# Optimization experiments

Hardware: AMD Instinct MI355X
Metric: run time of the kernel (lower is better)

## Reference

```python
import jax, jax.numpy as jnp
import numpy as np

D = 1024

def setup_inputs() -> dict:
    key = jax.random.key(0)
    ks = jax.random.split(key, 7)
    s = 1.0 / np.sqrt(D)
    x = jax.random.normal(ks[0], (4, 4096, D), dtype=jnp.float32)
    Wq = jax.random.uniform(ks[1], (D, D), jnp.float32, -s, s)
    bq = jax.random.uniform(ks[2], (D,), jnp.float32, -s, s)
    Wk = jax.random.uniform(ks[3], (D, D), jnp.float32, -s, s)
    bk = jax.random.uniform(ks[4], (D,), jnp.float32, -s, s)
    Wv = jax.random.uniform(ks[5], (D, D), jnp.float32, -s, s)
    bv = jax.random.uniform(ks[6], (D,), jnp.float32, -s, s)
    return {"x": x, "Wq": Wq, "bq": bq, "Wk": Wk, "bk": bk, "Wv": Wv, "bv": bv}

def reference(x, Wq, bq, Wk, bk, Wv, bv):
    # nn.Linear: y = x @ W.T + b
    q = (jnp.einsum('bnd,ed->bne', x, Wq) + bq) / jnp.sqrt(jnp.float32(Wq.shape[0]))
    k = jnp.einsum('bnd,ed->bne', x, Wk) + bk
    v = jnp.einsum('bnd,ed->bne', x, Wv) + bv
    scores = jnp.einsum('bqd,bkd->bqk', q, k)  # [B,N,N]
    N = scores.shape[-1]
    mask = jnp.triu(jnp.full((N, N), -1e9, dtype=scores.dtype), k=1)
    probs = jax.nn.softmax(scores + mask, axis=-1)
    return jnp.einsum('bqk,bkd->bqd', probs, v)
```

## Files before the change

kernel.cpp:

```cpp
#include <hip/hip_runtime.h>
#include <hip/hip_bf16.h>
#include <stdint.h>


typedef __attribute__((ext_vector_type(8))) short short8;
typedef __attribute__((ext_vector_type(4))) float float4v;

__device__ inline unsigned short f2b(float f) {
  union { float f; unsigned u; } v; v.f = f;
  unsigned r = (v.u + 0x7fffu + ((v.u >> 16) & 1u)) >> 16;
  return (unsigned short)r;
}
__device__ inline float b2f(unsigned short b) {
  union { unsigned u; float f; } v; v.u = ((unsigned)b) << 16;
  return v.f;
}

typedef const __attribute__((address_space(1))) unsigned int* gptr_t;
typedef __attribute__((address_space(3))) unsigned int* lptr_t;

__device__ inline void gload_lds16(const unsigned short* g, unsigned short* l) {
  __builtin_amdgcn_global_load_lds((gptr_t)(const void*)g, (lptr_t)(void*)l, 16, 0, 0);
}

__global__ __launch_bounds__(256) void cvt_all(const float* __restrict__ x,
                                               const float* __restrict__ wq,
                                               const float* __restrict__ wk,
                                               const float* __restrict__ wv,
                                               unsigned short* __restrict__ xb,
                                               unsigned short* __restrict__ wb) {
  const float* src;
  unsigned short* dst;
  long n, i0, stride;
  if (blockIdx.x < 2048) {
    src = x; dst = xb; n = 16384L * 1024;
    i0 = ((long)blockIdx.x * 256 + threadIdx.x) * 4;
    stride = 2048L * 256 * 4;
  } else {
    int wsec = (blockIdx.x - 2048) >> 8;
    int blk = (blockIdx.x - 2048) & 255;
    src = wsec == 0 ? wq : (wsec == 1 ? wk : wv);
    dst = wb + (long)wsec * 1024 * 1024;
    n = 1024L * 1024;
    i0 = ((long)blk * 256 + threadIdx.x) * 4;
    stride = 256L * 256 * 4;
  }
  for (long i = i0; i < n; i += stride) {
    float4 f = *(const float4*)&src[i];
    union { unsigned short u[4]; uint2 v; } o;
    o.u[0] = f2b(f.x); o.u[1] = f2b(f.y); o.u[2] = f2b(f.z); o.u[3] = f2b(f.w);
    *(uint2*)&dst[i] = o.v;
  }
}

__device__ __forceinline__ void stage_half(const unsigned short* __restrict__ g,
                                           int grow0, int tile, int kk,
                                           char* tb, int tid) {
  const int kc = tile * 64 + kk * 32;
#pragma unroll
  for (int j = 0; j < 2; j++) {
    int c = j * 512 + tid;
    int lc = c ^ ((c >> 3) & 3);
    gload_lds16(g + (long)(grow0 + (lc >> 2)) * 1024 + kc + (lc & 3) * 8,
                (unsigned short*)(tb + kk * 16384 + (j * 512 + (tid & 448)) * 16));
  }
}

#define DSA(dst, TB, kk, mi) do { \
  int o = (kk) * 16384 + (wr * 128 + (mi) * 16 + lr) * 64 + g16; \
  o ^= ((o >> 3) & 0x30); dst = *(const short8*)((TB) + o); } while (0)
#define DSB(dst, TB, kk, ni) do { \
  int o = (kk) * 16384 + (wc * 64 + (ni) * 16 + lr) * 64 + g16; \
  o ^= ((o >> 3) & 0x30); dst = *(const short8*)((TB) + o); } while (0)

#define MF(x, y, z) __builtin_amdgcn_mfma_f32_16x16x32_bf16(x, y, z, 0, 0, 0)
#define MMQ(M0) \
  acc[M0 + 0][0] = MF(a0, b0, acc[M0 + 0][0]); \
  acc[M0 + 0][1] = MF(a0, b1, acc[M0 + 0][1]); \
  acc[M0 + 0][2] = MF(a0, b2, acc[M0 + 0][2]); \
  acc[M0 + 0][3] = MF(a0, b3, acc[M0 + 0][3]); \
  acc[M0 + 1][0] = MF(a1, b0, acc[M0 + 1][0]); \
  acc[M0 + 1][1] = MF(a1, b1, acc[M0 + 1][1]); \
  acc[M0 + 1][2] = MF(a1, b2, acc[M0 + 1][2]); \
  acc[M0 + 1][3] = MF(a1, b3, acc[M0 + 1][3]); \
  acc[M0 + 2][0] = MF(a2, b0, acc[M0 + 2][0]); \
  acc[M0 + 2][1] = MF(a2, b1, acc[M0 + 2][1]); \
  acc[M0 + 2][2] = MF(a2, b2, acc[M0 + 2][2]); \
  acc[M0 + 2][3] = MF(a2, b3, acc[M0 + 2][3]); \
  acc[M0 + 3][0] = MF(a3, b0, acc[M0 + 3][0]); \
  acc[M0 + 3][1] = MF(a3, b1, acc[M0 + 3][1]); \
  acc[M0 + 3][2] = MF(a3, b2, acc[M0 + 3][2]); \
  acc[M0 + 3][3] = MF(a3, b3, acc[M0 + 3][3]);

#define KTILE(AT, BT, OA, t) do { \
  short8 a0, a1, a2, a3, b0, b1, b2, b3; \
  DSB(b0, BT, 0, 0); DSB(b1, BT, 0, 1); DSB(b2, BT, 0, 2); DSB(b3, BT, 0, 3); \
  DSA(a0, AT, 0, 0); DSA(a1, AT, 0, 1); DSA(a2, AT, 0, 2); DSA(a3, AT, 0, 3); \
  if ((t) + 1 < NT) stage_half(A, rowA0, (t) + 1, 1, OA, tid); \
  __builtin_amdgcn_s_barrier(); \
  __builtin_amdgcn_s_setprio(1); MMQ(0); __builtin_amdgcn_s_setprio(0); \
  __builtin_amdgcn_s_barrier(); \
  DSA(a0, AT, 0, 4); DSA(a1, AT, 0, 5); DSA(a2, AT, 0, 6); DSA(a3, AT, 0, 7); \
  if ((t) + 2 < NT) stage_half(Bm, rowB0, (t) + 2, 0, BT, tid); \
  __builtin_amdgcn_s_barrier(); \
  __builtin_amdgcn_s_setprio(1); MMQ(4); __builtin_amdgcn_s_setprio(0); \
  __builtin_amdgcn_s_barrier(); \
  DSB(b0, BT, 1, 0); DSB(b1, BT, 1, 1); DSB(b2, BT, 1, 2); DSB(b3, BT, 1, 3); \
  DSA(a0, AT, 1, 0); DSA(a1, AT, 1, 1); DSA(a2, AT, 1, 2); DSA(a3, AT, 1, 3); \
  if ((t) + 2 < NT) stage_half(A, rowA0, (t) + 2, 0, AT, tid); \
  __builtin_amdgcn_s_barrier(); \
  __builtin_amdgcn_s_setprio(1); MMQ(0); __builtin_amdgcn_s_setprio(0); \
  __builtin_amdgcn_s_barrier(); \
  DSA(a0, AT, 1, 4); DSA(a1, AT, 1, 5); DSA(a2, AT, 1, 6); DSA(a3, AT, 1, 7); \
  if ((t) + 2 < NT) stage_half(Bm, rowB0, (t) + 2, 1, BT, tid); \
  __builtin_amdgcn_s_barrier(); \
  __builtin_amdgcn_s_setprio(1); MMQ(4); __builtin_amdgcn_s_setprio(0); \
  if ((t) + 2 < NT) { asm volatile("s_waitcnt vmcnt(6)" ::: "memory"); } \
  else               { asm volatile("s_waitcnt vmcnt(0)" ::: "memory"); } \
  __builtin_amdgcn_s_barrier(); \
} while (0)

template <int MODE>
__global__ __launch_bounds__(512, 2) void gemm8p(
    const unsigned short* __restrict__ Ag, const unsigned short* __restrict__ Bg,
    const float* __restrict__ b0v, const float* __restrict__ b1v,
    const float* __restrict__ b2v, void* __restrict__ Cg,
    long sA, long sB, long sC) {
  __shared__ __align__(16) char smem[131072];
  const int NT = 16;

  int bi, bj, b;
  if (MODE == 0) {
    bi = blockIdx.x; bj = blockIdx.y; b = 0;
  } else {
    int t = blockIdx.x % 136;
    b = blockIdx.x / 136;
    int r = (int)((sqrtf(8.0f * t + 1.0f) - 1.0f) * 0.5f);
    while ((r + 1) * (r + 2) / 2 <= t) r++;
    while (r * (r + 1) / 2 > t) r--;
    bi = r; bj = t - r * (r + 1) / 2;
  }

  const unsigned short* A = Ag + (long)b * sA;
  const unsigned short* Bm = Bg + (long)b * sB;

  const int tid = threadIdx.x;
  const int l = tid & 63, w = tid >> 6;
  const int wr = w >> 2, wc = w & 3;
  const int lr = l & 15, g16 = (l >> 4) * 16;
  const int rowA0 = bi * 256, rowB0 = bj * 256;

  char* A0 = smem;
  char* B0 = smem + 32768;
  char* A1 = smem + 65536;
  char* B1 = smem + 98304;

  float4v acc[8][4];
#pragma unroll
  for (int i = 0; i < 8; i++)
#pragma unroll
    for (int j = 0; j < 4; j++) acc[i][j] = (float4v){0.f, 0.f, 0.f, 0.f};

  stage_half(A, rowA0, 0, 0, A0, tid);
  stage_half(Bm, rowB0, 0, 0, B0, tid);
  stage_half(A, rowA0, 0, 1, A0, tid);
  stage_half(Bm, rowB0, 0, 1, B0, tid);
  stage_half(Bm, rowB0, 1, 0, B1, tid);
  stage_half(A, rowA0, 1, 0, A1, tid);
  stage_half(Bm, rowB0, 1, 1, B1, tid);
  asm volatile("s_waitcnt vmcnt(6)" ::: "memory");
  __builtin_amdgcn_s_barrier();

#pragma unroll 1
  for (int t = 0; t < NT; t += 2) {
    KTILE(A0, B0, A1, t);
    KTILE(A1, B1, A0, t + 1);
  }

  if (MODE == 0) {
    const int sec = bj >> 2;
    const float* bias = sec == 0 ? b0v : (sec == 1 ? b1v : b2v);
    const float scale = sec == 0 ? 0.03125f : 1.0f;
    unsigned short* C = (unsigned short*)Cg + (long)sec * 16777216L;
    const int colbase = (bj & 3) * 256 + wc * 64;
#pragma unroll
    for (int mi = 0; mi < 8; mi++) {
      int rbase = bi * 256 + wr * 128 + mi * 16 + (l >> 4) * 4;
#pragma unroll
      for (int ni = 0; ni < 4; ni++) {
        int col = colbase + ni * 16 + lr;
        float bb = bias[col];
#pragma unroll
        for (int j = 0; j < 4; j++)
          C[(long)(rbase + j) * 1024 + col] = f2b((acc[mi][ni][j] + bb) * scale);
      }
    }
  } else {
    unsigned short* C = (unsigned short*)Cg + (long)b * sC;
#pragma unroll
    for (int mi = 0; mi < 8; mi++) {
      int rbase = bi * 256 + wr * 128 + mi * 16 + (l >> 4) * 4;
#pragma unroll
      for (int ni = 0; ni < 4; ni++) {
        int col = bj * 256 + wc * 64 + ni * 16 + lr;
#pragma unroll
        for (int j = 0; j < 4; j++)
          C[(long)(rbase + j) * 4096 + col] = f2b(acc[mi][ni][j]);
      }
    }
  }
}


__device__ __forceinline__ void pv_src(int tt, int NT1, int bi, int bi2,
                                       int* ar, int* kc) {
  if (tt < NT1) { *ar = bi << 8; *kc = tt << 6; }
  else          { *ar = bi2 << 8; *kc = (tt - NT1) << 6; }
}

__device__ __forceinline__ void pv_stageA(const unsigned short* __restrict__ g,
                                          int ar, int kc, int kk, char* tb, int tid) {
#pragma unroll
  for (int j = 0; j < 2; j++) {
    int c = j * 512 + tid;
    int lc = c ^ ((c >> 3) & 3);
    gload_lds16(g + (long)(ar + (lc >> 2)) * 4096 + kc + kk * 32 + (lc & 3) * 8,
                (unsigned short*)(tb + kk * 16384 + (j * 512 + (tid & 448)) * 16));
  }
}

__device__ __forceinline__ void pv_stageB(const unsigned short* __restrict__ g,
                                          int br, int kc, char* tb, int tid) {
#pragma unroll
  for (int kk = 0; kk < 2; kk++) {
    int lc = tid ^ ((tid >> 3) & 3);
    gload_lds16(g + (long)(br + (lc >> 2)) * 4096 + kc + kk * 32 + (lc & 3) * 8,
                (unsigned short*)(tb + kk * 8192 + (tid & 448) * 16));
  }
}

#define PDSA(dst, TB, kk, mi) do { \
  int o = (kk) * 16384 + (wr * 64 + (mi) * 16 + lr) * 64 + g16; \
  o ^= ((o >> 3) & 0x30); dst = *(const short8*)((TB) + o); } while (0)
#define PDSB(dst, TB, kk, ni) do { \
  int o = (kk) * 8192 + (wc * 64 + (ni) * 16 + lr) * 64 + g16; \
  o ^= ((o >> 3) & 0x30); dst = *(const short8*)((TB) + o); } while (0)

#define PMM \
  acc[0][0] = MF(a0, b0, acc[0][0]); acc[0][1] = MF(a0, b1, acc[0][1]); \
  acc[0][2] = MF(a0, b2, acc[0][2]); acc[0][3] = MF(a0, b3, acc[0][3]); \
  acc[1][0] = MF(a1, b0, acc[1][0]); acc[1][1] = MF(a1, b1, acc[1][1]); \
  acc[1][2] = MF(a1, b2, acc[1][2]); acc[1][3] = MF(a1, b3, acc[1][3]); \
  acc[2][0] = MF(a2, b0, acc[2][0]); acc[2][1] = MF(a2, b1, acc[2][1]); \
  acc[2][2] = MF(a2, b2, acc[2][2]); acc[2][3] = MF(a2, b3, acc[2][3]); \
  acc[3][0] = MF(a3, b0, acc[3][0]); acc[3][1] = MF(a3, b1, acc[3][1]); \
  acc[3][2] = MF(a3, b2, acc[3][2]); acc[3][3] = MF(a3, b3, acc[3][3]);

#define PVTILE(CA, CB, OA, OB, t) do { \
  short8 a0, a1, a2, a3, b0, b1, b2, b3; \
  PDSB(b0, CB, 0, 0); PDSB(b1, CB, 0, 1); PDSB(b2, CB, 0, 2); PDSB(b3, CB, 0, 3); \
  PDSA(a0, CA, 0, 0); PDSA(a1, CA, 0, 1); PDSA(a2, CA, 0, 2); PDSA(a3, CA, 0, 3); \
  if ((t) + 1 < 68) { \
    int ar_, kc_; pv_src((t) + 1, NT1, bi, bi2, &ar_, &kc_); \
    pv_stageA(Sb, ar_, kc_, 1, OA, tid); \
    pv_stageB(vTb, brow0, kc_, OB, tid); \
  } \
  __builtin_amdgcn_s_barrier(); \
  __builtin_amdgcn_s_setprio(1); PMM; __builtin_amdgcn_s_setprio(0); \
  __builtin_amdgcn_s_barrier(); \
  PDSB(b0, CB, 1, 0); PDSB(b1, CB, 1, 1); PDSB(b2, CB, 1, 2); PDSB(b3, CB, 1, 3); \
  PDSA(a0, CA, 1, 0); PDSA(a1, CA, 1, 1); PDSA(a2, CA, 1, 2); PDSA(a3, CA, 1, 3); \
  if ((t) + 2 < 68) { \
    int ar_, kc_; pv_src((t) + 2, NT1, bi, bi2, &ar_, &kc_); \
    pv_stageA(Sb, ar_, kc_, 0, CA, tid); \
  } \
  __builtin_amdgcn_s_barrier(); \
  __builtin_amdgcn_s_setprio(1); PMM; __builtin_amdgcn_s_setprio(0); \
  if ((t) + 2 < 68) { asm volatile("s_waitcnt vmcnt(2)" ::: "memory"); } \
  else              { asm volatile("s_waitcnt vmcnt(0)" ::: "memory"); } \
  __builtin_amdgcn_s_barrier(); \
} while (0)

#define PV_STORE(row0) do { \
  float* C = Cg + (long)b * 4194304L; \
  _Pragma("unroll") for (int mi = 0; mi < 4; mi++) { \
    int rbase = (row0) + wr * 64 + mi * 16 + (l >> 4) * 4; \
    _Pragma("unroll") for (int ni = 0; ni < 4; ni++) { \
      int col = brow0 + wc * 64 + ni * 16 + lr; \
      _Pragma("unroll") for (int j = 0; j < 4; j++) \
        C[(long)(rbase + j) * 1024 + col] = acc[mi][ni][j]; \
    } \
  } \
} while (0)

__global__ __launch_bounds__(512, 2) void pv8p(const unsigned short* __restrict__ Sg,
                                               const unsigned short* __restrict__ vTg,
                                               float* __restrict__ Cg) {
  __shared__ __align__(16) char smem[98304];
  const int bi = blockIdx.x;
  const int bj = blockIdx.y;
  const int b = blockIdx.z;
  const int bi2 = 15 - bi;
  const int NT1 = 4 * (bi + 1);

  const unsigned short* Sb = Sg + (long)b * 16777216L;
  const unsigned short* vTb = vTg + (long)b * 4194304L;
  const int brow0 = bj * 128;

  const int tid = threadIdx.x;
  const int l = tid & 63, w = tid >> 6;
  const int wr = w >> 1, wc = w & 1;
  const int lr = l & 15, g16 = (l >> 4) * 16;

  char* XA = smem;
  char* YA = smem + 32768;
  char* XB = smem + 65536;
  char* YB = smem + 81920;

  float4v acc[4][4];
#pragma unroll
  for (int i = 0; i < 4; i++)
#pragma unroll
    for (int j = 0; j < 4; j++) acc[i][j] = (float4v){0.f, 0.f, 0.f, 0.f};

  {
    int ar_, kc_;
    pv_src(0, NT1, bi, bi2, &ar_, &kc_);
    pv_stageA(Sb, ar_, kc_, 0, XA, tid);
    pv_stageA(Sb, ar_, kc_, 1, XA, tid);
    pv_stageB(vTb, brow0, kc_, XB, tid);
    pv_src(1, NT1, bi, bi2, &ar_, &kc_);
    pv_stageA(Sb, ar_, kc_, 0, YA, tid);
  }
  asm volatile("s_waitcnt vmcnt(2)" ::: "memory");
  __builtin_amdgcn_s_barrier();

#pragma unroll 1
  for (int t = 0; t < 68; t += 2) {
    if (t == NT1) {
      PV_STORE(bi * 256);
#pragma unroll
      for (int i = 0; i < 4; i++)
#pragma unroll
        for (int j = 0; j < 4; j++) acc[i][j] = (float4v){0.f, 0.f, 0.f, 0.f};
    }
    PVTILE(XA, XB, YA, YB, t);
    PVTILE(YA, YB, XA, XB, t + 1);
  }
  PV_STORE(bi2 * 256);
}

__global__ __launch_bounds__(256) void softmax_causal(unsigned short* __restrict__ S) {
  const int bid = blockIdx.x;
  const int b = bid >> 12, i = bid & 4095;
  unsigned short* row = S + ((long)b * 4096 + i) * 4096;
  const int len = i + 1;
  const int padTo = ((i >> 8) + 1) << 8;
  const int nch = padTo >> 3;
  const int tid = threadIdx.x;
  const int w = tid >> 6;

  float v[2][8];
  int nc[2];
  float m = -3e38f;
#pragma unroll
  for (int s = 0; s < 2; s++) {
    int c = tid + s * 256;
    nc[s] = -1;
    if (c < nch) {
      nc[s] = c;
      short8 x = *(const short8*)&row[c * 8];
#pragma unroll
      for (int j = 0; j < 8; j++) {
        int idx = c * 8 + j;
        float f = (idx < len) ? b2f((unsigned short)x[j]) : -3e38f;
        v[s][j] = f;
        m = fmaxf(m, f);
      }
    }
  }

  __shared__ float red[4];
#pragma unroll
  for (int off = 32; off; off >>= 1) m = fmaxf(m, __shfl_xor(m, off));
  if ((tid & 63) == 0) red[w] = m;
  __syncthreads();
  m = fmaxf(fmaxf(red[0], red[1]), fmaxf(red[2], red[3]));

  float sum = 0.f;
#pragma unroll
  for (int s = 0; s < 2; s++) {
    if (nc[s] >= 0) {
#pragma unroll
      for (int j = 0; j < 8; j++) {
        float e = __expf(v[s][j] - m);
        v[s][j] = e;
        sum += e;
      }
    }
  }
  __syncthreads();
#pragma unroll
  for (int off = 32; off; off >>= 1) sum += __shfl_xor(sum, off);
  if ((tid & 63) == 0) red[w] = sum;
  __syncthreads();
  sum = red[0] + red[1] + red[2] + red[3];
  const float inv = 1.0f / sum;

#pragma unroll
  for (int s = 0; s < 2; s++) {
    if (nc[s] >= 0) {
      int c = nc[s];
      short8 o;
#pragma unroll
      for (int j = 0; j < 8; j++) o[j] = (short)f2b(v[s][j] * inv);
      *(short8*)&row[c * 8] = o;
    }
  }
}

__global__ __launch_bounds__(256) void transpose_v(const unsigned short* __restrict__ V,
                                                   unsigned short* __restrict__ VT) {
  __shared__ unsigned short t[64][65];
  const int b = blockIdx.z;
  const int n0 = blockIdx.x * 64;
  const int d0 = blockIdx.y * 64;
  const unsigned short* Vb = V + (long)b * 4096 * 1024;
  unsigned short* VTb = VT + (long)b * 1024 * 4096;
  const int tid = threadIdx.x;
#pragma unroll
  for (int s = 0; s < 2; s++) {
    int c = s * 256 + tid;
    int r = c >> 3, c8 = (c & 7) * 8;
    short8 x = *(const short8*)&Vb[(long)(n0 + r) * 1024 + d0 + c8];
#pragma unroll
    for (int j = 0; j < 8; j++) t[r][c8 + j] = (unsigned short)x[j];
  }
  __syncthreads();
#pragma unroll
  for (int s = 0; s < 2; s++) {
    int c = s * 256 + tid;
    int dr = c >> 3, n8 = (c & 7) * 8;
    short8 o;
#pragma unroll
    for (int j = 0; j < 8; j++) o[j] = (short)t[n8 + j][dr];
    *(short8*)&VTb[(long)(d0 + dr) * 4096 + n0 + n8] = o;
  }
}

extern "C" void kernel_launch(void* const* d_in, const int* in_sizes, int n_in,
                              void* d_out, int out_size, void* d_ws, size_t ws_size,
                              hipStream_t stream) {
  const float* x  = (const float*)d_in[0];
  const float* Wq = (const float*)d_in[1];
  const float* bq = (const float*)d_in[2];
  const float* Wk = (const float*)d_in[3];
  const float* bk = (const float*)d_in[4];
  const float* Wv = (const float*)d_in[5];
  const float* bv = (const float*)d_in[6];
  float* out = (float*)d_out;

  const long NTOK = 16384L;
  const long D = 1024L;
  const long NB = 4096L;

  unsigned short* ws = (unsigned short*)d_ws;
  unsigned short* qb = ws;
  unsigned short* kb = qb + NTOK * D;
  unsigned short* vb = kb + NTOK * D;
  unsigned short* vT = vb + NTOK * D;
  unsigned short* S  = vT + NTOK * D;
  unsigned short* xb  = S;
  unsigned short* Wb  = S + NTOK * D;

  cvt_all<<<2048 + 3 * 256, 256, 0, stream>>>(x, Wq, Wk, Wv, xb, Wb);

  gemm8p<0><<<dim3(64, 12), 512, 0, stream>>>(xb, Wb, bq, bk, bv, qb, 0, 0, 0);

  transpose_v<<<dim3(64, 16, 4), 256, 0, stream>>>(vb, vT);

  gemm8p<1><<<544, 512, 0, stream>>>(qb, kb, nullptr, nullptr, nullptr, S,
      NB * D, NB * D, NB * NB);

  softmax_causal<<<16384, 256, 0, stream>>>(S);

  pv8p<<<dim3(8, 8, 4), 512, 0, stream>>>(S, vT, out);
}
```

Measured before the change: 448.9 us.

## Register-prefetch LDS fragments and drop half the barriers in GEMM and PV loops

Restructures the GEMM k-tile loop so LDS fragments for the next MFMA group are read into named registers while the current group computes. The next tile's first fragments are also prefetched across the loop boundary, and about half of the s_barriers are removed in both the QKV/score GEMM and the PV kernel. Swizzled LDS addresses are now precomputed once per thread as base offsets, so the per-load XOR arithmetic goes away. The aim is to hide LDS latency and cut barrier stalls, at the cost of more VGPRs (a risk to the two-blocks-per-CU occupancy) and a more delicate ordering between the restaged buffers and the fragment reads.

```diff
diff --git a/kernel.cpp b/kernel.cpp
--- a/kernel.cpp
+++ b/kernel.cpp
@@ -66,57 +66,54 @@
   }
 }
 
-#define DSA(dst, TB, kk, mi) do { \
-  int o = (kk) * 16384 + (wr * 128 + (mi) * 16 + lr) * 64 + g16; \
-  o ^= ((o >> 3) & 0x30); dst = *(const short8*)((TB) + o); } while (0)
-#define DSB(dst, TB, kk, ni) do { \
-  int o = (kk) * 16384 + (wc * 64 + (ni) * 16 + lr) * 64 + g16; \
-  o ^= ((o >> 3) & 0x30); dst = *(const short8*)((TB) + o); } while (0)
+#define LDA(dst, TB, kk, mi) dst = *(const short8*)((TB) + baseA + (kk) * 16384 + (mi) * 1024)
+#define LDB(dst, TB, kk, ni) dst = *(const short8*)((TB) + baseB + (kk) * 16384 + (ni) * 1024)
 
 #define MF(x, y, z) __builtin_amdgcn_mfma_f32_16x16x32_bf16(x, y, z, 0, 0, 0)
-#define MMQ(M0) \
-  acc[M0 + 0][0] = MF(a0, b0, acc[M0 + 0][0]); \
-  acc[M0 + 0][1] = MF(a0, b1, acc[M0 + 0][1]); \
-  acc[M0 + 0][2] = MF(a0, b2, acc[M0 + 0][2]); \
-  acc[M0 + 0][3] = MF(a0, b3, acc[M0 + 0][3]); \
-  acc[M0 + 1][0] = MF(a1, b0, acc[M0 + 1][0]); \
-  acc[M0 + 1][1] = MF(a1, b1, acc[M0 + 1][1]); \
-  acc[M0 + 1][2] = MF(a1, b2, acc[M0 + 1][2]); \
-  acc[M0 + 1][3] = MF(a1, b3, acc[M0 + 1][3]); \
-  acc[M0 + 2][0] = MF(a2, b0, acc[M0 + 2][0]); \
-  acc[M0 + 2][1] = MF(a2, b1, acc[M0 + 2][1]); \
-  acc[M0 + 2][2] = MF(a2, b2, acc[M0 + 2][2]); \
-  acc[M0 + 2][3] = MF(a2, b3, acc[M0 + 2][3]); \
-  acc[M0 + 3][0] = MF(a3, b0, acc[M0 + 3][0]); \
-  acc[M0 + 3][1] = MF(a3, b1, acc[M0 + 3][1]); \
-  acc[M0 + 3][2] = MF(a3, b2, acc[M0 + 3][2]); \
-  acc[M0 + 3][3] = MF(a3, b3, acc[M0 + 3][3]);
-
-#define KTILE(AT, BT, OA, t) do { \
-  short8 a0, a1, a2, a3, b0, b1, b2, b3; \
-  DSB(b0, BT, 0, 0); DSB(b1, BT, 0, 1); DSB(b2, BT, 0, 2); DSB(b3, BT, 0, 3); \
-  DSA(a0, AT, 0, 0); DSA(a1, AT, 0, 1); DSA(a2, AT, 0, 2); DSA(a3, AT, 0, 3); \
+#define MM4x4(x0, x1, x2, x3, y0, y1, y2, y3, M0) \
+  acc[M0 + 0][0] = MF(x0, y0, acc[M0 + 0][0]); \
+  acc[M0 + 0][1] = MF(x0, y1, acc[M0 + 0][1]); \
+  acc[M0 + 0][2] = MF(x0, y2, acc[M0 + 0][2]); \
+  acc[M0 + 0][3] = MF(x0, y3, acc[M0 + 0][3]); \
+  acc[M0 + 1][0] = MF(x1, y0, acc[M0 + 1][0]); \
+  acc[M0 + 1][1] = MF(x1, y1, acc[M0 + 1][1]); \
+  acc[M0 + 1][2] = MF(x1, y2, acc[M0 + 1][2]); \
+  acc[M0 + 1][3] = MF(x1, y3, acc[M0 + 1][3]); \
+  acc[M0 + 2][0] = MF(x2, y0, acc[M0 + 2][0]); \
+  acc[M0 + 2][1] = MF(x2, y1, acc[M0 + 2][1]); \
+  acc[M0 + 2][2] = MF(x2, y2, acc[M0 + 2][2]); \
+  acc[M0 + 2][3] = MF(x2, y3, acc[M0 + 2][3]); \
+  acc[M0 + 3][0] = MF(x3, y0, acc[M0 + 3][0]); \
+  acc[M0 + 3][1] = MF(x3, y1, acc[M0 + 3][1]); \
+  acc[M0 + 3][2] = MF(x3, y2, acc[M0 + 3][2]); \
+  acc[M0 + 3][3] = MF(x3, y3, acc[M0 + 3][3]);
+
+#define KTILE_RA(CA, CB, OA, OB, t) do { \
+   \
+  LDA(A4r, CA, 0, 4); LDA(A5r, CA, 0, 5); LDA(A6r, CA, 0, 6); LDA(A7r, CA, 0, 7); \
   if ((t) + 1 < NT) stage_half(A, rowA0, (t) + 1, 1, OA, tid); \
-  __builtin_amdgcn_s_barrier(); \
-  __builtin_amdgcn_s_setprio(1); MMQ(0); __builtin_amdgcn_s_setprio(0); \
-  __builtin_amdgcn_s_barrier(); \
-  DSA(a0, AT, 0, 4); DSA(a1, AT, 0, 5); DSA(a2, AT, 0, 6); DSA(a3, AT, 0, 7); \
-  if ((t) + 2 < NT) stage_half(Bm, rowB0, (t) + 2, 0, BT, tid); \
-  __builtin_amdgcn_s_barrier(); \
-  __builtin_amdgcn_s_setprio(1); MMQ(4); __builtin_amdgcn_s_setprio(0); \
-  __builtin_amdgcn_s_barrier(); \
-  DSB(b0, BT, 1, 0); DSB(b1, BT, 1, 1); DSB(b2, BT, 1, 2); DSB(b3, BT, 1, 3); \
-  DSA(a0, AT, 1, 0); DSA(a1, AT, 1, 1); DSA(a2, AT, 1, 2); DSA(a3, AT, 1, 3); \
-  if ((t) + 2 < NT) stage_half(A, rowA0, (t) + 2, 0, AT, tid); \
-  __builtin_amdgcn_s_barrier(); \
-  __builtin_amdgcn_s_setprio(1); MMQ(0); __builtin_amdgcn_s_setprio(0); \
-  __builtin_amdgcn_s_barrier(); \
-  DSA(a0, AT, 1, 4); DSA(a1, AT, 1, 5); DSA(a2, AT, 1, 6); DSA(a3, AT, 1, 7); \
-  if ((t) + 2 < NT) stage_half(Bm, rowB0, (t) + 2, 1, BT, tid); \
-  __builtin_amdgcn_s_barrier(); \
-  __builtin_amdgcn_s_setprio(1); MMQ(4); __builtin_amdgcn_s_setprio(0); \
-  if ((t) + 2 < NT) { asm volatile("s_waitcnt vmcnt(6)" ::: "memory"); } \
-  else               { asm volatile("s_waitcnt vmcnt(0)" ::: "memory"); } \
+  __builtin_amdgcn_s_setprio(1); MM4x4(A0r, A1r, A2r, A3r, B00, B01, B02, B03, 0); __builtin_amdgcn_s_setprio(0); \
+  __builtin_amdgcn_s_barrier(); \
+   \
+  LDB(B10, CB, 1, 0); LDB(B11, CB, 1, 1); LDB(B12, CB, 1, 2); LDB(B13, CB, 1, 3); \
+  LDA(A0r, CA, 1, 0); LDA(A1r, CA, 1, 1); LDA(A2r, CA, 1, 2); LDA(A3r, CA, 1, 3); \
+  if ((t) + 2 < NT) stage_half(Bm, rowB0, (t) + 2, 0, CB, tid); \
+  __builtin_amdgcn_s_setprio(1); MM4x4(A4r, A5r, A6r, A7r, B00, B01, B02, B03, 4); __builtin_amdgcn_s_setprio(0); \
+  __builtin_amdgcn_s_barrier(); \
+   \
+  LDA(A4r, CA, 1, 4); LDA(A5r, CA, 1, 5); LDA(A6r, CA, 1, 6); LDA(A7r, CA, 1, 7); \
+  if ((t) + 2 < NT) stage_half(A, rowA0, (t) + 2, 0, CA, tid); \
+  __builtin_amdgcn_s_setprio(1); MM4x4(A0r, A1r, A2r, A3r, B10, B11, B12, B13, 0); __builtin_amdgcn_s_setprio(0); \
+  __builtin_amdgcn_s_barrier(); \
+   \
+  if ((t) + 1 < NT) { \
+    if ((t) + 2 < NT) { asm volatile("s_waitcnt vmcnt(4)" ::: "memory"); } \
+    else              { asm volatile("s_waitcnt vmcnt(0)" ::: "memory"); } \
+    LDB(B00, OB, 0, 0); LDB(B01, OB, 0, 1); LDB(B02, OB, 0, 2); LDB(B03, OB, 0, 3); \
+    LDA(A0r, OA, 0, 0); LDA(A1r, OA, 0, 1); LDA(A2r, OA, 0, 2); LDA(A3r, OA, 0, 3); \
+  } \
+  if ((t) + 2 < NT) stage_half(Bm, rowB0, (t) + 2, 1, CB, tid); \
+  __builtin_amdgcn_s_setprio(1); MM4x4(A4r, A5r, A6r, A7r, B10, B11, B12, B13, 4); __builtin_amdgcn_s_setprio(0); \
   __builtin_amdgcn_s_barrier(); \
 } while (0)
 
@@ -149,6 +146,9 @@
   const int wr = w >> 2, wc = w & 3;
   const int lr = l & 15, g16 = (l >> 4) * 16;
   const int rowA0 = bi * 256, rowB0 = bj * 256;
+  const int laneswz = lr * 64 + (g16 ^ (((lr >> 1) & 3) << 4));
+  const int baseA = wr * 8192 + laneswz;
+  const int baseB = wc * 4096 + laneswz;
 
   char* A0 = smem;
   char* B0 = smem + 32768;
@@ -171,10 +171,15 @@
   asm volatile("s_waitcnt vmcnt(6)" ::: "memory");
   __builtin_amdgcn_s_barrier();
 
+  short8 A0r, A1r, A2r, A3r, A4r, A5r, A6r, A7r;
+  short8 B00, B01, B02, B03, B10, B11, B12, B13;
+  LDB(B00, B0, 0, 0); LDB(B01, B0, 0, 1); LDB(B02, B0, 0, 2); LDB(B03, B0, 0, 3);
+  LDA(A0r, A0, 0, 0); LDA(A1r, A0, 0, 1); LDA(A2r, A0, 0, 2); LDA(A3r, A0, 0, 3);
+
 #pragma unroll 1
   for (int t = 0; t < NT; t += 2) {
-    KTILE(A0, B0, A1, t);
-    KTILE(A1, B1, A0, t + 1);
+    KTILE_RA(A0, B0, A1, B1, t);
+    KTILE_RA(A1, B1, A0, B0, t + 1);
   }
 
   if (MODE == 0) {
@@ -211,7 +216,6 @@
   }
 }
 
-
 __device__ __forceinline__ void pv_src(int tt, int NT1, int bi, int bi2,
                                        int* ar, int* kc) {
   if (tt < NT1) { *ar = bi << 8; *kc = tt << 6; }
@@ -239,43 +243,36 @@
   }
 }
 
-#define PDSA(dst, TB, kk, mi) do { \
-  int o = (kk) * 16384 + (wr * 64 + (mi) * 16 + lr) * 64 + g16; \
-  o ^= ((o >> 3) & 0x30); dst = *(const short8*)((TB) + o); } while (0)
-#define PDSB(dst, TB, kk, ni) do { \
-  int o = (kk) * 8192 + (wc * 64 + (ni) * 16 + lr) * 64 + g16; \
-  o ^= ((o >> 3) & 0x30); dst = *(const short8*)((TB) + o); } while (0)
-
-#define PMM \
-  acc[0][0] = MF(a0, b0, acc[0][0]); acc[0][1] = MF(a0, b1, acc[0][1]); \
-  acc[0][2] = MF(a0, b2, acc[0][2]); acc[0][3] = MF(a0, b3, acc[0][3]); \
-  acc[1][0] = MF(a1, b0, acc[1][0]); acc[1][1] = MF(a1, b1, acc[1][1]); \
-  acc[1][2] = MF(a1, b2, acc[1][2]); acc[1][3] = MF(a1, b3, acc[1][3]); \
-  acc[2][0] = MF(a2, b0, acc[2][0]); acc[2][1] = MF(a2, b1, acc[2][1]); \
-  acc[2][2] = MF(a2, b2, acc[2][2]); acc[2][3] = MF(a2, b3, acc[2][3]); \
-  acc[3][0] = MF(a3, b0, acc[3][0]); acc[3][1] = MF(a3, b1, acc[3][1]); \
-  acc[3][2] = MF(a3, b2, acc[3][2]); acc[3][3] = MF(a3, b3, acc[3][3]);
-
-#define PVTILE(CA, CB, OA, OB, t) do { \
-  short8 a0, a1, a2, a3, b0, b1, b2, b3; \
-  PDSB(b0, CB, 0, 0); PDSB(b1, CB, 0, 1); PDSB(b2, CB, 0, 2); PDSB(b3, CB, 0, 3); \
-  PDSA(a0, CA, 0, 0); PDSA(a1, CA, 0, 1); PDSA(a2, CA, 0, 2); PDSA(a3, CA, 0, 3); \
+#define LDPA(dst, TB, kk, mi) dst = *(const short8*)((TB) + basePA + (kk) * 16384 + (mi) * 1024)
+#define LDPB(dst, TB, kk, ni) dst = *(const short8*)((TB) + basePB + (kk) * 8192 + (ni) * 1024)
+
+#define PMMX(x0, x1, x2, x3, y0, y1, y2, y3) \
+  acc[0][0] = MF(x0, y0, acc[0][0]); acc[0][1] = MF(x0, y1, acc[0][1]); \
+  acc[0][2] = MF(x0, y2, acc[0][2]); acc[0][3] = MF(x0, y3, acc[0][3]); \
+  acc[1][0] = MF(x1, y0, acc[1][0]); acc[1][1] = MF(x1, y1, acc[1][1]); \
+  acc[1][2] = MF(x1, y2, acc[1][2]); acc[1][3] = MF(x1, y3, acc[1][3]); \
+  acc[2][0] = MF(x2, y0, acc[2][0]); acc[2][1] = MF(x2, y1, acc[2][1]); \
+  acc[2][2] = MF(x2, y2, acc[2][2]); acc[2][3] = MF(x2, y3, acc[2][3]); \
+  acc[3][0] = MF(x3, y0, acc[3][0]); acc[3][1] = MF(x3, y1, acc[3][1]); \
+  acc[3][2] = MF(x3, y2, acc[3][2]); acc[3][3] = MF(x3, y3, acc[3][3]);
+
+#define PVTILE_RA(CA, CB, OA, OB, t) do { \
+  LDPB(PB00, CB, 0, 0); LDPB(PB01, CB, 0, 1); LDPB(PB02, CB, 0, 2); LDPB(PB03, CB, 0, 3); \
+  LDPA(PA00, CA, 0, 0); LDPA(PA01, CA, 0, 1); LDPA(PA02, CA, 0, 2); LDPA(PA03, CA, 0, 3); \
+  LDPB(PB10, CB, 1, 0); LDPB(PB11, CB, 1, 1); LDPB(PB12, CB, 1, 2); LDPB(PB13, CB, 1, 3); \
+  LDPA(PA10, CA, 1, 0); LDPA(PA11, CA, 1, 1); LDPA(PA12, CA, 1, 2); LDPA(PA13, CA, 1, 3); \
   if ((t) + 1 < 68) { \
     int ar_, kc_; pv_src((t) + 1, NT1, bi, bi2, &ar_, &kc_); \
     pv_stageA(Sb, ar_, kc_, 1, OA, tid); \
     pv_stageB(vTb, brow0, kc_, OB, tid); \
   } \
-  __builtin_amdgcn_s_barrier(); \
-  __builtin_amdgcn_s_setprio(1); PMM; __builtin_amdgcn_s_setprio(0); \
-  __builtin_amdgcn_s_barrier(); \
-  PDSB(b0, CB, 1, 0); PDSB(b1, CB, 1, 1); PDSB(b2, CB, 1, 2); PDSB(b3, CB, 1, 3); \
-  PDSA(a0, CA, 1, 0); PDSA(a1, CA, 1, 1); PDSA(a2, CA, 1, 2); PDSA(a3, CA, 1, 3); \
+  __builtin_amdgcn_s_setprio(1); PMMX(PA00, PA01, PA02, PA03, PB00, PB01, PB02, PB03); __builtin_amdgcn_s_setprio(0); \
+  __builtin_amdgcn_s_barrier(); \
   if ((t) + 2 < 68) { \
     int ar_, kc_; pv_src((t) + 2, NT1, bi, bi2, &ar_, &kc_); \
     pv_stageA(Sb, ar_, kc_, 0, CA, tid); \
   } \
-  __builtin_amdgcn_s_barrier(); \
-  __builtin_amdgcn_s_setprio(1); PMM; __builtin_amdgcn_s_setprio(0); \
+  __builtin_amdgcn_s_setprio(1); PMMX(PA10, PA11, PA12, PA13, PB10, PB11, PB12, PB13); __builtin_amdgcn_s_setprio(0); \
   if ((t) + 2 < 68) { asm volatile("s_waitcnt vmcnt(2)" ::: "memory"); } \
   else              { asm volatile("s_waitcnt vmcnt(0)" ::: "memory"); } \
   __builtin_amdgcn_s_barrier(); \
@@ -311,6 +308,9 @@
   const int l = tid & 63, w = tid >> 6;
   const int wr = w >> 1, wc = w & 1;
   const int lr = l & 15, g16 = (l >> 4) * 16;
+  const int laneswz = lr * 64 + (g16 ^ (((lr >> 1) & 3) << 4));
+  const int basePA = wr * 4096 + laneswz;
+  const int basePB = wc * 4096 + laneswz;
 
   char* XA = smem;
   char* YA = smem + 32768;
@@ -335,6 +335,9 @@
   asm volatile("s_waitcnt vmcnt(2)" ::: "memory");
   __builtin_amdgcn_s_barrier();
 
+  short8 PA00, PA01, PA02, PA03, PA10, PA11, PA12, PA13;
+  short8 PB00, PB01, PB02, PB03, PB10, PB11, PB12, PB13;
+
 #pragma unroll 1
   for (int t = 0; t < 68; t += 2) {
     if (t == NT1) {
@@ -344,8 +347,8 @@
 #pragma unroll
         for (int j = 0; j < 4; j++) acc[i][j] = (float4v){0.f, 0.f, 0.f, 0.f};
     }
-    PVTILE(XA, XB, YA, YB, t);
-    PVTILE(YA, YB, XA, XB, t + 1);
+    PVTILE_RA(XA, XB, YA, YB, t);
+    PVTILE_RA(YA, YB, XA, XB, t + 1);
   }
   PV_STORE(bi2 * 256);
 }
```

New measurement: 693.5 us. 54.5% more time.

## Fuse V transpose into QKV GEMM epilogue and swizzle block order for XCDs

Applied to the files above, without the earlier changes.

The QKV projection GEMM now writes the V section directly in transposed layout (d-major, token-contiguous) from its epilogue, so the separate transpose_v kernel and its extra read/write pass over V are removed. Both GEMM launches also remap the linear block index so that consecutive tiles land on the same XCD (index mod 8 interleave), aiming for better L2 reuse of shared A/B tiles. The transposed epilogue writes 8-byte strided chunks, which may coalesce less well than the row-major stores.

```diff
diff --git a/kernel.cpp b/kernel.cpp
--- a/kernel.cpp
+++ b/kernel.cpp
@@ -125,16 +125,19 @@
     const unsigned short* __restrict__ Ag, const unsigned short* __restrict__ Bg,
     const float* __restrict__ b0v, const float* __restrict__ b1v,
     const float* __restrict__ b2v, void* __restrict__ Cg,
+    unsigned short* __restrict__ vTout,
     long sA, long sB, long sC) {
   __shared__ __align__(16) char smem[131072];
   const int NT = 16;
 
   int bi, bj, b;
   if (MODE == 0) {
-    bi = blockIdx.x; bj = blockIdx.y; b = 0;
+    int swz = (blockIdx.x & 7) * 96 + (blockIdx.x >> 3);
+    bi = swz / 12; bj = swz % 12; b = 0;
   } else {
-    int t = blockIdx.x % 136;
-    b = blockIdx.x / 136;
+    int swz = (blockIdx.x & 7) * 68 + (blockIdx.x >> 3);
+    b = swz / 136;
+    int t = swz % 136;
     int r = (int)((sqrtf(8.0f * t + 1.0f) - 1.0f) * 0.5f);
     while ((r + 1) * (r + 2) / 2 <= t) r++;
     while (r * (r + 1) / 2 > t) r--;
@@ -180,19 +183,37 @@
   if (MODE == 0) {
     const int sec = bj >> 2;
     const float* bias = sec == 0 ? b0v : (sec == 1 ? b1v : b2v);
-    const float scale = sec == 0 ? 0.03125f : 1.0f;
-    unsigned short* C = (unsigned short*)Cg + (long)sec * 16777216L;
     const int colbase = (bj & 3) * 256 + wc * 64;
-#pragma unroll
-    for (int mi = 0; mi < 8; mi++) {
-      int rbase = bi * 256 + wr * 128 + mi * 16 + (l >> 4) * 4;
-#pragma unroll
-      for (int ni = 0; ni < 4; ni++) {
-        int col = colbase + ni * 16 + lr;
-        float bb = bias[col];
-#pragma unroll
-        for (int j = 0; j < 4; j++)
-          C[(long)(rbase + j) * 1024 + col] = f2b((acc[mi][ni][j] + bb) * scale);
+    if (sec < 2) {
+      const float scale = sec == 0 ? 0.03125f : 1.0f;
+      unsigned short* C = (unsigned short*)Cg + (long)sec * 16777216L;
+#pragma unroll
+      for (int mi = 0; mi < 8; mi++) {
+        int rbase = bi * 256 + wr * 128 + mi * 16 + (l >> 4) * 4;
+#pragma unroll
+        for (int ni = 0; ni < 4; ni++) {
+          int col = colbase + ni * 16 + lr;
+          float bb = bias[col];
+#pragma unroll
+          for (int j = 0; j < 4; j++)
+            C[(long)(rbase + j) * 1024 + col] = f2b((acc[mi][ni][j] + bb) * scale);
+        }
+      }
+    } else {
+#pragma unroll
+      for (int mi = 0; mi < 8; mi++) {
+        int rbase = bi * 256 + wr * 128 + mi * 16 + (l >> 4) * 4;
+        int bb = rbase >> 12;
+        int n0 = rbase & 4095;
+#pragma unroll
+        for (int ni = 0; ni < 4; ni++) {
+          int d = colbase + ni * 16 + lr;
+          float bv = bias[d];
+          union { unsigned short u[4]; uint2 v; } o;
+#pragma unroll
+          for (int j = 0; j < 4; j++) o.u[j] = f2b(acc[mi][ni][j] + bv);
+          *(uint2*)&vTout[(long)bb * 4194304L + (long)d * 4096 + n0] = o.v;
+        }
       }
     }
   } else {
@@ -210,7 +231,6 @@
     }
   }
 }
-
 
 __device__ __forceinline__ void pv_src(int tt, int NT1, int bi, int bi2,
                                        int* ar, int* kc) {
@@ -419,35 +439,6 @@
   }
 }
 
-__global__ __launch_bounds__(256) void transpose_v(const unsigned short* __restrict__ V,
-                                                   unsigned short* __restrict__ VT) {
-  __shared__ unsigned short t[64][65];
-  const int b = blockIdx.z;
-  const int n0 = blockIdx.x * 64;
-  const int d0 = blockIdx.y * 64;
-  const unsigned short* Vb = V + (long)b * 4096 * 1024;
-  unsigned short* VTb = VT + (long)b * 1024 * 4096;
-  const int tid = threadIdx.x;
-#pragma unroll
-  for (int s = 0; s < 2; s++) {
-    int c = s * 256 + tid;
-    int r = c >> 3, c8 = (c & 7) * 8;
-    short8 x = *(const short8*)&Vb[(long)(n0 + r) * 1024 + d0 + c8];
-#pragma unroll
-    for (int j = 0; j < 8; j++) t[r][c8 + j] = (unsigned short)x[j];
-  }
-  __syncthreads();
-#pragma unroll
-  for (int s = 0; s < 2; s++) {
-    int c = s * 256 + tid;
-    int dr = c >> 3, n8 = (c & 7) * 8;
-    short8 o;
-#pragma unroll
-    for (int j = 0; j < 8; j++) o[j] = (short)t[n8 + j][dr];
-    *(short8*)&VTb[(long)(d0 + dr) * 4096 + n0 + n8] = o;
-  }
-}
-
 extern "C" void kernel_launch(void* const* d_in, const int* in_sizes, int n_in,
                               void* d_out, int out_size, void* d_ws, size_t ws_size,
                               hipStream_t stream) {
@@ -475,12 +466,10 @@
 
   cvt_all<<<2048 + 3 * 256, 256, 0, stream>>>(x, Wq, Wk, Wv, xb, Wb);
 
-  gemm8p<0><<<dim3(64, 12), 512, 0, stream>>>(xb, Wb, bq, bk, bv, qb, 0, 0, 0);
-
-  transpose_v<<<dim3(64, 16, 4), 256, 0, stream>>>(vb, vT);
+  gemm8p<0><<<768, 512, 0, stream>>>(xb, Wb, bq, bk, bv, qb, vT, 0, 0, 0);
 
   gemm8p<1><<<544, 512, 0, stream>>>(qb, kb, nullptr, nullptr, nullptr, S,
-      NB * D, NB * D, NB * NB);
+      nullptr, NB * D, NB * D, NB * NB);
 
   softmax_causal<<<16384, 256, 0, stream>>>(S);
 
```

Measured after the change: 433.7 us. 1.04x faster.
